# Kernel tuning notes

Measured on AMD Instinct MI355X. Metric: run time of the kernel, lower is better.

Reference implementation:

```python
import jax, jax.numpy as jnp
import numpy as np
import math

N_HEAD = 16
HEAD_DIM = 64
LN_EPS = 1e-5
TEMP = 1.0

def _layernorm(x, scale, bias):
    # normalize over last dim (head_dim)
    mu = jnp.mean(x, axis=-1, keepdims=True)
    var = jnp.mean(jnp.square(x - mu), axis=-1, keepdims=True)
    return (x - mu) / jnp.sqrt(var + LN_EPS) * scale + bias

def setup_inputs() -> dict:
    key = jax.random.key(0)
    ks = jax.random.split(key, 3)
    B, S, C = 4, 2048, 1024
    x = jax.random.normal(ks[0], (B, S, C), dtype=jnp.float32)
    w_qkv = jax.random.normal(ks[1], (C, 3 * C), dtype=jnp.float32) * (C ** -0.5)
    w_proj = jax.random.normal(ks[2], (C, C), dtype=jnp.float32) * (C ** -0.5)
    return {
        "x": x,
        "w_qkv": w_qkv,
        "w_proj": w_proj,
        "q_scale": jnp.ones((HEAD_DIM,), jnp.float32),
        "q_bias": jnp.zeros((HEAD_DIM,), jnp.float32),
        "k_scale": jnp.ones((HEAD_DIM,), jnp.float32),
        "k_bias": jnp.zeros((HEAD_DIM,), jnp.float32),
    }

def reference(x, w_qkv, w_proj, q_scale, q_bias, k_scale, k_bias):
    B, S, C = x.shape
    H, D = N_HEAD, HEAD_DIM
    # qkv projection -> [B,S,3,H,D] -> [3,B,H,S,D]
    qkv = (x @ w_qkv).reshape(B, S, 3, H, D).transpose(2, 0, 3, 1, 4)
    q = _layernorm(qkv[0], q_scale, q_bias)
    k = _layernorm(qkv[1], k_scale, k_bias)
    v = qkv[2]
    # temperature-scaled logits, stable softmax
    inv = 1.0 / (math.sqrt(D) * max(TEMP, 1e-6))
    logits = jnp.einsum('bhqd,bhkd->bhqk', q, k) * inv
    att = jax.nn.softmax(logits, axis=-1)
    # entropy stats (track_stats=True path)
    s_raw = -jnp.sum(att * jnp.log(att + 1e-9), axis=-1)  # [B,H,S]
    batch_entropies = jnp.mean(s_raw / math.log(S), axis=(1, 2))  # [B]
    out = jnp.einsum('bhqk,bhkd->bhqd', att, v).transpose(0, 2, 1, 3).reshape(B, S, C)
    return out @ w_proj, batch_entropies
```

## Files before the change

kernel.cpp:

```cpp
#include <hip/hip_runtime.h>
#include <hip/hip_bf16.h>
#include <math.h>

#define CB 4
#define CS 2048
#define CC 1024
#define CH 16
#define CD 64
#define CBS (CB*CS)

typedef unsigned short u16;
typedef __bf16 bf16x8 __attribute__((ext_vector_type(8)));
typedef float f32x4 __attribute__((ext_vector_type(4)));
typedef float f32x16 __attribute__((ext_vector_type(16)));
typedef unsigned short u16x4 __attribute__((ext_vector_type(4)));
typedef unsigned short u16x8 __attribute__((ext_vector_type(8)));
typedef unsigned u32x2 __attribute__((ext_vector_type(2)));

__device__ __forceinline__ u16 f2bf(float f){
  union { float f; unsigned u; } v; v.f = f;
  unsigned r = v.u + 0x7FFFu + ((v.u >> 16) & 1u);
  return (u16)(r >> 16);
}
__device__ __forceinline__ unsigned pack2bf(float a, float b){
  __hip_bfloat162 h = __float22bfloat162_rn(make_float2(a, b));
  union { __hip_bfloat162 h; unsigned u; } c; c.h = h; return c.u;
}
__device__ __forceinline__ f32x4 mfma16(bf16x8 a, bf16x8 b, f32x4 c){
  return __builtin_amdgcn_mfma_f32_16x16x32_bf16(a, b, c, 0, 0, 0);
}
__device__ __forceinline__ f32x16 mfma32(bf16x8 a, bf16x8 b, f32x16 c){
  return __builtin_amdgcn_mfma_f32_32x32x16_bf16(a, b, c, 0, 0, 0);
}
__device__ __forceinline__ void gload16(const u16* g, u16* lds_base_uniform){
  __builtin_amdgcn_global_load_lds(
      (const __attribute__((address_space(1))) unsigned int*)g,
      (__attribute__((address_space(3))) unsigned int*)lds_base_uniform, 16, 0, 0);
}

__global__ __launch_bounds__(256) void convert_x_kernel(
    const float* __restrict__ x, u16* __restrict__ xb, float* __restrict__ zero4){
  if (blockIdx.x == 0 && threadIdx.x < 4) zero4[threadIdx.x] = 0.0f;
  size_t i = ((size_t)blockIdx.x*256 + threadIdx.x)*8;
  float4 a = *(const float4*)(x+i);
  float4 b = *(const float4*)(x+i+4);
  u16x8 o = { f2bf(a.x),f2bf(a.y),f2bf(a.z),f2bf(a.w),
              f2bf(b.x),f2bf(b.y),f2bf(b.z),f2bf(b.w) };
  *(u16x8*)(xb+i) = o;
}

template<int K, int N>
__global__ __launch_bounds__(256) void transpose_convert_kernel(
    const float* __restrict__ w, u16* __restrict__ wt){
  __shared__ u16 tile[64][65];
  const int nb = N/64;
  int tk0 = (blockIdx.x / nb) * 64;
  int tn0 = (blockIdx.x % nb) * 64;
  int t = threadIdx.x;
  for (int i = 0; i < 4; i++) {
    int r = i*16 + (t>>4);
    int c = (t&15)*4;
    float4 v = *(const float4*)(w + (size_t)(tk0+r)*N + tn0 + c);
    tile[c+0][r]=f2bf(v.x); tile[c+1][r]=f2bf(v.y);
    tile[c+2][r]=f2bf(v.z); tile[c+3][r]=f2bf(v.w);
  }
  __syncthreads();
  for (int i = 0; i < 4; i++) {
    int r = i*16 + (t>>4);
    int c = (t&15)*4;
    u16x4 o = { tile[r][c+0], tile[r][c+1], tile[r][c+2], tile[r][c+3] };
    *(u16x4*)(wt + (size_t)(tn0+r)*K + tk0 + c) = o;
  }
}

__global__ __launch_bounds__(256) void transpose_v_kernel(
    const u16* __restrict__ vb, u16* __restrict__ vtb){
  __shared__ u16 tile[64][72];
  int bh = blockIdx.x >> 5;
  int st = blockIdx.x & 31;
  int t = threadIdx.x;
  const u16* src = vb + (size_t)bh*CS*CD + (size_t)st*64*CD;
  int r = t>>2, c = (t&3)*16;
  *(u16x8*)&tile[r][c]   = *(const u16x8*)(src + (size_t)r*CD + c);
  *(u16x8*)&tile[r][c+8] = *(const u16x8*)(src + (size_t)r*CD + c + 8);
  __syncthreads();
  int d = t>>2, s = (t&3)*16;
  u16x8 o0, o1;
  for (int j=0;j<8;j++){ o0[j] = tile[s+j][d]; o1[j] = tile[s+8+j][d]; }
  u16* dst = vtb + (size_t)bh*CD*CS + (size_t)d*CS + st*64 + s;
  *(u16x8*)dst = o0;
  *(u16x8*)(dst+8) = o1;
}

__global__ __launch_bounds__(256, 3) void gemm_qkv_ln_kernel(
    const u16* __restrict__ xb, const u16* __restrict__ wqkvT,
    const float* __restrict__ qsc, const float* __restrict__ qbi,
    const float* __restrict__ ksc, const float* __restrict__ kbi,
    u16* __restrict__ qb, u16* __restrict__ kb, u16* __restrict__ vb){
  __shared__ __align__(16) u16 bl[3][128*32];
  int t = threadIdx.x;
  int wv = t >> 6, lane = t & 63, lo = lane & 15, q4 = lane >> 4;
  int m0 = blockIdx.x * 128;
  int n0 = blockIdx.y * 128;
  int lsB = (lane & 3) ^ ((lane >> 3) & 3);
  const u16* bg0  = wqkvT + (size_t)(n0 + (lane>>2))*CC + lsB*8;
  const u16* agl0 = xb + (size_t)(m0 + wv*32 + lo)*CC + q4*8;
  const u16* agl1 = agl0 + (size_t)16*CC;

  f32x4 acc[2][8];
  #pragma unroll
  for (int i=0;i<2;i++)
    #pragma unroll
    for (int j=0;j<8;j++) acc[i][j] = (f32x4){0.f,0.f,0.f,0.f};

  auto stageB = [&](int buf, int kk){
    #pragma unroll
    for (int cc=0; cc<2; cc++){
      int c = wv*2 + cc;
      gload16(bg0 + (size_t)c*16*CC + kk*32, &bl[buf][c*512]);
    }
  };

  stageB(0, 0);
  stageB(1, 1);
  bf16x8 acur0 = *(const bf16x8*)(agl0);
  bf16x8 acur1 = *(const bf16x8*)(agl1);
  int cur = 0;
  const int akey = (lo >> 1) & 3;

  for (int kk = 0; kk < 32; kk++){
    if (kk < 30){
      asm volatile("s_waitcnt vmcnt(4)" ::: "memory");
      __builtin_amdgcn_s_barrier();
      __builtin_amdgcn_sched_barrier(0);
      int nb = cur + 2; if (nb >= 3) nb -= 3;
      stageB(nb, kk + 2);
    } else if (kk == 30){
      asm volatile("s_waitcnt vmcnt(4)" ::: "memory");
      __builtin_amdgcn_s_barrier();
      __builtin_amdgcn_sched_barrier(0);
    } else {
      asm volatile("s_waitcnt vmcnt(0)" ::: "memory");
      __builtin_amdgcn_s_barrier();
      __builtin_amdgcn_sched_barrier(0);
    }
    bf16x8 anxt0, anxt1;
    if (kk < 31){
      anxt0 = *(const bf16x8*)(agl0 + (kk+1)*32);
      anxt1 = *(const bf16x8*)(agl1 + (kk+1)*32);
    } else {
      anxt0 = acur0; anxt1 = acur1;
    }
    const u16* bc = &bl[cur][0];
    int soff = (q4 ^ akey) << 3;
    __builtin_amdgcn_s_setprio(1);
    #pragma unroll
    for (int nt=0; nt<8; nt++){
      bf16x8 b = *(const bf16x8*)&bc[(nt*16 + lo)*32 + soff];
      acc[0][nt] = mfma16(acur0, b, acc[0][nt]);
      acc[1][nt] = mfma16(acur1, b, acc[1][nt]);
    }
    __builtin_amdgcn_s_setprio(0);
    acur0 = anxt0; acur1 = anxt1;
    cur = (cur == 2) ? 0 : cur + 1;
  }

  int three = n0 >> 10;
  int h0 = (n0 & 1023) >> 6;
  const float* scp = (three == 0) ? qsc : ksc;
  const float* bip = (three == 0) ? qbi : kbi;
  float outscale = (three == 0) ? 0.125f * 1.44269504088896f : 1.0f;
  u16* dst = (three == 0) ? qb : (three == 1 ? kb : vb);

  for (int rt = 0; rt < 2; rt++){
    int tg = m0 + wv*32 + rt*16 + q4*4;
    for (int hf = 0; hf < 2; hf++){
      int h = h0 + hf;
      for (int r = 0; r < 4; r++){
        int token = tg + r;
        int bb = token >> 11, ss = token & (CS-1);
        size_t base = (((size_t)(bb*CH + h))*CS + ss)*CD;
        if (three < 2){
          float s1 = 0.f, s2 = 0.f;
          for (int j=0;j<4;j++){ float v = acc[rt][hf*4+j][r]; s1 += v; s2 += v*v; }
          for (int off=8; off>=1; off>>=1){
            s1 += __shfl_xor(s1, off, 16);
            s2 += __shfl_xor(s2, off, 16);
          }
          float mean = s1 * (1.f/64.f);
          float var  = s2 * (1.f/64.f) - mean*mean;
          float rstd = rsqrtf(var + 1e-5f);
          for (int j=0;j<4;j++){
            int d = j*16 + lo;
            float v = (acc[rt][hf*4+j][r] - mean) * rstd * scp[d] + bip[d];
            dst[base + d] = f2bf(v * outscale);
          }
        } else {
          for (int j=0;j<4;j++){
            int d = j*16 + lo;
            dst[base + d] = f2bf(acc[rt][hf*4+j][r]);
          }
        }
      }
    }
  }
}

__global__ __launch_bounds__(256, 2) void attention_kernel(
    const u16* __restrict__ qb, const u16* __restrict__ kb,
    const u16* __restrict__ vtb, u16* __restrict__ attnb, float* __restrict__ ent){
  __shared__ __align__(16) u16 kl[3][32*64];
  __shared__ __align__(16) u16 vl[3][64*32];
  int t = threadIdx.x;
  int wv = t >> 6, lane = t & 63;
  int col = lane & 31, hi = lane >> 5;
  int n = blockIdx.x;
  int xc = n & 7, j = n >> 3;
  int bh = xc + 8*(j >> 4);
  int qt = j & 15;
  int bI = bh >> 4;
  int q0w = qt*128 + wv*32;
  const u16* qbp = qb  + (size_t)bh * CS * CD;
  const u16* kbp = kb  + (size_t)bh * CS * CD;
  const u16* vbp = vtb + (size_t)bh * CD * CS;

  int srow8  = lane >> 3, sl8 = lane & 7;
  int srow16 = lane >> 2, sl4 = lane & 3;

  bf16x8 qf[4];
  #pragma unroll
  for (int ks=0;ks<4;ks++)
    qf[ks] = *(const bf16x8*)(qbp + (size_t)(q0w + col)*CD + ks*16 + hi*8);

  f32x16 o[2];
  #pragma unroll
  for (int nt=0;nt<2;nt++)
    #pragma unroll
    for (int i=0;i<16;i++) o[nt][i] = 0.f;
  float zacc = 0.f, tacc = 0.f;

  auto stage = [&](int buf, int tile){
    int skn = tile*32;
    int krow  = wv*8 + srow8;
    int kslot = sl8 ^ srow8 ^ wv;
    gload16(kbp + (size_t)(skn + krow)*CD + kslot*8, &kl[buf][wv*512]);
    int vrow  = wv*16 + srow16;
    int vslot = sl4 ^ (srow16 & 3);
    gload16(vbp + (size_t)vrow*CS + skn + vslot*8, &vl[buf][wv*512]);
  };

  stage(0, 0);
  stage(1, 1);

  const int kkey = (col & 7) ^ (col >> 3);
  const int vkey = (col & 3);
  int cur = 0;

  for (int it = 0; it < 64; it++){
    if (it < 62){
      asm volatile("s_waitcnt vmcnt(2)" ::: "memory");
      __builtin_amdgcn_s_barrier();
      __builtin_amdgcn_sched_barrier(0);
      int nb = cur + 2; if (nb >= 3) nb -= 3;
      stage(nb, it + 2);
    } else if (it == 62){
      asm volatile("s_waitcnt vmcnt(2)" ::: "memory");
      __builtin_amdgcn_s_barrier();
      __builtin_amdgcn_sched_barrier(0);
    } else {
      asm volatile("s_waitcnt vmcnt(0)" ::: "memory");
      __builtin_amdgcn_s_barrier();
      __builtin_amdgcn_sched_barrier(0);
    }
    const u16* kc = &kl[cur][0];
    const u16* vc = &vl[cur][0];

    bf16x8 kfr[4], vfr[2][2];
    #pragma unroll
    for (int ks=0;ks<4;ks++)
      kfr[ks] = *(const bf16x8*)&kc[col*64 + (((2*ks+hi) ^ kkey)<<3)];
    #pragma unroll
    for (int nt=0;nt<2;nt++)
      #pragma unroll
      for (int ks=0;ks<2;ks++)
        vfr[nt][ks] = *(const bf16x8*)&vc[(nt*32+col)*32 + (((ks*2+hi) ^ vkey)<<3)];

    f32x16 sf;
    #pragma unroll
    for (int i=0;i<16;i++) sf[i] = 0.f;
    __builtin_amdgcn_s_setprio(1);
    #pragma unroll
    for (int ks=0;ks<4;ks++)
      sf = mfma32(kfr[ks], qf[ks], sf);
    __builtin_amdgcn_s_setprio(0);

    #pragma unroll
    for (int ksl=0; ksl<2; ksl++){
      float p[2][4];
      #pragma unroll
      for (int gg=0; gg<2; gg++){
        int g = 2*ksl + gg;
        float l0 = sf[g*4+0], l1 = sf[g*4+1],
              l2 = sf[g*4+2], l3 = sf[g*4+3];
        float p0 = __builtin_amdgcn_exp2f(l0);
        float p1 = __builtin_amdgcn_exp2f(l1);
        float p2 = __builtin_amdgcn_exp2f(l2);
        float p3 = __builtin_amdgcn_exp2f(l3);
        zacc += (p0+p1)+(p2+p3);
        tacc += (p0*l0+p1*l1)+(p2*l2+p3*l3);
        p[gg][0]=p0; p[gg][1]=p1; p[gg][2]=p2; p[gg][3]=p3;
      }
      unsigned x0 = pack2bf(p[0][0], p[0][1]);
      unsigned x1 = pack2bf(p[0][2], p[0][3]);
      unsigned y0 = pack2bf(p[1][0], p[1][1]);
      unsigned y1 = pack2bf(p[1][2], p[1][3]);
      u32x2 s0 = __builtin_amdgcn_permlane32_swap(x0, y0, false, false);
      u32x2 s1 = __builtin_amdgcn_permlane32_swap(x1, y1, false, false);
      union { unsigned u[4]; bf16x8 v; } ap;
      ap.u[0] = s0[0]; ap.u[1] = s1[0]; ap.u[2] = s0[1]; ap.u[3] = s1[1];
      __builtin_amdgcn_s_setprio(1);
      o[0] = mfma32(ap.v, vfr[0][ksl], o[0]);
      o[1] = mfma32(ap.v, vfr[1][ksl], o[1]);
      __builtin_amdgcn_s_setprio(0);
    }
    cur = (cur == 2) ? 0 : cur + 1;
  }

  float z2 = zacc + __shfl_xor(zacc, 32);
  float t2 = tacc + __shfl_xor(tacc, 32);
  float invz = 1.f / z2;

  float srowv = 0.69314718055995f * (__builtin_amdgcn_logf(z2) - t2 * invz);
  float ev = (hi == 0) ? srowv : 0.f;
  for (int off=1; off<=32; off<<=1) ev += __shfl_xor(ev, off);
  if (lane == 0){
    float entscale = 1.0f / ((float)CH * (float)CS * logf((float)CS));
    atomicAdd(&ent[bI], ev * entscale);
  }

  float izv[4][4];
  #pragma unroll
  for (int g=0; g<4; g++)
    #pragma unroll
    for (int r=0; r<4; r++)
      izv[g][r] = __shfl(invz, 8*g + 4*hi + r);

  u16* obase = attnb + ((size_t)bh*CS + q0w)*CD;
  #pragma unroll
  for (int nt=0;nt<2;nt++){
    #pragma unroll
    for (int g=0;g<4;g++){
      #pragma unroll
      for (int r=0;r<4;r++){
        int qrow = 8*g + 4*hi + r;
        obase[(size_t)qrow*CD + nt*32 + col] = f2bf(o[nt][g*4+r] * izv[g][r]);
      }
    }
  }
}

__global__ __launch_bounds__(256, 3) void gemm_out_kernel(
    const u16* __restrict__ attnH, const u16* __restrict__ wprojT,
    float* __restrict__ out){
  __shared__ __align__(16) u16 bl[3][128*32];
  int t = threadIdx.x;
  int wv = t >> 6, lane = t & 63, lo = lane & 15, q4 = lane >> 4;
  int m0 = blockIdx.x * 128;
  int n0 = blockIdx.y * 128;
  int b  = m0 >> 11, s0 = m0 & (CS-1);
  int lsB = (lane & 3) ^ ((lane >> 3) & 3);
  const u16* bg0 = wprojT + (size_t)(n0 + (lane>>2))*CC + lsB*8;
  const u16* agl0 = attnH + ((size_t)(b*CH)*CS + s0 + wv*32 + lo)*CD + q4*8;
  const u16* agl1 = agl0 + (size_t)16*CD;

  f32x4 acc[2][8];
  #pragma unroll
  for (int i=0;i<2;i++)
    #pragma unroll
    for (int j=0;j<8;j++) acc[i][j] = (f32x4){0.f,0.f,0.f,0.f};

  auto aoff = [&](int kk) -> size_t {
    return (size_t)(kk >> 1)*CS*CD + (size_t)(kk & 1)*32;
  };
  auto stageB = [&](int buf, int kk){
    #pragma unroll
    for (int cc=0; cc<2; cc++){
      int c = wv*2 + cc;
      gload16(bg0 + (size_t)c*16*CC + kk*32, &bl[buf][c*512]);
    }
  };

  stageB(0, 0);
  stageB(1, 1);
  bf16x8 acur0 = *(const bf16x8*)(agl0);
  bf16x8 acur1 = *(const bf16x8*)(agl1);
  int cur = 0;
  const int akey = (lo >> 1) & 3;

  for (int kk = 0; kk < 32; kk++){
    if (kk < 30){
      asm volatile("s_waitcnt vmcnt(4)" ::: "memory");
      __builtin_amdgcn_s_barrier();
      __builtin_amdgcn_sched_barrier(0);
      int nb = cur + 2; if (nb >= 3) nb -= 3;
      stageB(nb, kk + 2);
    } else if (kk == 30){
      asm volatile("s_waitcnt vmcnt(4)" ::: "memory");
      __builtin_amdgcn_s_barrier();
      __builtin_amdgcn_sched_barrier(0);
    } else {
      asm volatile("s_waitcnt vmcnt(0)" ::: "memory");
      __builtin_amdgcn_s_barrier();
      __builtin_amdgcn_sched_barrier(0);
    }
    bf16x8 anxt0, anxt1;
    if (kk < 31){
      size_t ao = aoff(kk + 1);
      anxt0 = *(const bf16x8*)(agl0 + ao);
      anxt1 = *(const bf16x8*)(agl1 + ao);
    } else {
      anxt0 = acur0; anxt1 = acur1;
    }
    const u16* bc = &bl[cur][0];
    int soff = (q4 ^ akey) << 3;
    __builtin_amdgcn_s_setprio(1);
    #pragma unroll
    for (int nt=0; nt<8; nt++){
      bf16x8 b2 = *(const bf16x8*)&bc[(nt*16 + lo)*32 + soff];
      acc[0][nt] = mfma16(acur0, b2, acc[0][nt]);
      acc[1][nt] = mfma16(acur1, b2, acc[1][nt]);
    }
    __builtin_amdgcn_s_setprio(0);
    acur0 = anxt0; acur1 = anxt1;
    cur = (cur == 2) ? 0 : cur + 1;
  }

  for (int rt=0;rt<2;rt++){
    for (int r=0;r<4;r++){
      int row = m0 + wv*32 + rt*16 + q4*4 + r;
      for (int nt=0;nt<8;nt++)
        out[(size_t)row*CC + n0 + nt*16 + lo] = acc[rt][nt][r];
    }
  }
}

extern "C" void kernel_launch(void* const* d_in, const int* in_sizes, int n_in,
                              void* d_out, int out_size, void* d_ws, size_t ws_size,
                              hipStream_t stream) {
  const float* x      = (const float*)d_in[0];
  const float* w_qkv  = (const float*)d_in[1];
  const float* w_proj = (const float*)d_in[2];
  const float* q_scale= (const float*)d_in[3];
  const float* q_bias = (const float*)d_in[4];
  const float* k_scale= (const float*)d_in[5];
  const float* k_bias = (const float*)d_in[6];
  float* out = (float*)d_out;
  float* ent = out + (size_t)CBS * CC;

  u16* xb     = (u16*)d_ws;
  u16* wqkvT  = xb     + (size_t)CBS*CC;
  u16* wprojT = wqkvT  + (size_t)3*CC*CC;
  u16* qb     = wprojT + (size_t)CC*CC;
  u16* kb     = qb + (size_t)CB*CH*CS*CD;
  u16* vb     = kb + (size_t)CB*CH*CS*CD;
  u16* vbT    = xb;
  u16* attn   = vb;

  convert_x_kernel<<<dim3(CBS*CC/(256*8)), 256, 0, stream>>>(x, xb, ent);
  transpose_convert_kernel<CC, 3*CC><<<dim3((CC/64)*(3*CC/64)), 256, 0, stream>>>(w_qkv, wqkvT);
  transpose_convert_kernel<CC, CC><<<dim3((CC/64)*(CC/64)), 256, 0, stream>>>(w_proj, wprojT);
  gemm_qkv_ln_kernel<<<dim3(CBS/128, 3*CC/128), 256, 0, stream>>>(
      xb, wqkvT, q_scale, q_bias, k_scale, k_bias, qb, kb, vb);
  transpose_v_kernel<<<dim3(CB*CH*(CS/64)), 256, 0, stream>>>(vb, vbT);
  attention_kernel<<<dim3(CB*CH*(CS/128)), 256, 0, stream>>>(qb, kb, vbT, attn, ent);
  gemm_out_kernel<<<dim3(CBS/128, CC/128), 256, 0, stream>>>(attn, wprojT, out);
}
```

Baseline: 332.8 us.

## Enlarge GEMM M-tile to 256 rows per block in QKV and output projections

Both projection GEMMs now compute 256x128 tiles instead of 128x128, with each wave holding four 16-row A fragments and 4x8 accumulators. Each B tile staged in shared memory is reused across twice as many MFMAs, which cuts LDS B traffic and global B loads per FLOP. The waitcnt thresholds are adjusted for the extra in-flight A loads, and launch bounds drop to 2 blocks per CU to allow the higher register use. The grid is halved, which reduces occupancy and the number of blocks available to fill the GPU.

After: 347.5 us. 1.04x slower.

```diff
diff --git a/kernel.cpp b/kernel.cpp
--- a/kernel.cpp
+++ b/kernel.cpp
@@ -92,7 +92,7 @@
   *(u16x8*)(dst+8) = o1;
 }
 
-__global__ __launch_bounds__(256, 3) void gemm_qkv_ln_kernel(
+__global__ __launch_bounds__(256, 2) void gemm_qkv_ln_kernel(
     const u16* __restrict__ xb, const u16* __restrict__ wqkvT,
     const float* __restrict__ qsc, const float* __restrict__ qbi,
     const float* __restrict__ ksc, const float* __restrict__ kbi,
@@ -100,16 +100,18 @@
   __shared__ __align__(16) u16 bl[3][128*32];
   int t = threadIdx.x;
   int wv = t >> 6, lane = t & 63, lo = lane & 15, q4 = lane >> 4;
-  int m0 = blockIdx.x * 128;
+  int m0 = blockIdx.x * 256;
   int n0 = blockIdx.y * 128;
   int lsB = (lane & 3) ^ ((lane >> 3) & 3);
-  const u16* bg0  = wqkvT + (size_t)(n0 + (lane>>2))*CC + lsB*8;
-  const u16* agl0 = xb + (size_t)(m0 + wv*32 + lo)*CC + q4*8;
-  const u16* agl1 = agl0 + (size_t)16*CC;
-
-  f32x4 acc[2][8];
-  #pragma unroll
-  for (int i=0;i<2;i++)
+  const u16* bg0 = wqkvT + (size_t)(n0 + (lane>>2))*CC + lsB*8;
+  const u16* agl[4];
+  #pragma unroll
+  for (int g=0; g<4; g++)
+    agl[g] = xb + (size_t)(m0 + wv*64 + g*16 + lo)*CC + q4*8;
+
+  f32x4 acc[4][8];
+  #pragma unroll
+  for (int i=0;i<4;i++)
     #pragma unroll
     for (int j=0;j<8;j++) acc[i][j] = (f32x4){0.f,0.f,0.f,0.f};
 
@@ -123,33 +125,35 @@
 
   stageB(0, 0);
   stageB(1, 1);
-  bf16x8 acur0 = *(const bf16x8*)(agl0);
-  bf16x8 acur1 = *(const bf16x8*)(agl1);
+  bf16x8 acur[4];
+  #pragma unroll
+  for (int g=0; g<4; g++) acur[g] = *(const bf16x8*)(agl[g]);
   int cur = 0;
   const int akey = (lo >> 1) & 3;
 
   for (int kk = 0; kk < 32; kk++){
     if (kk < 30){
-      asm volatile("s_waitcnt vmcnt(4)" ::: "memory");
+      asm volatile("s_waitcnt vmcnt(6)" ::: "memory");
       __builtin_amdgcn_s_barrier();
       __builtin_amdgcn_sched_barrier(0);
       int nb = cur + 2; if (nb >= 3) nb -= 3;
       stageB(nb, kk + 2);
     } else if (kk == 30){
+      asm volatile("s_waitcnt vmcnt(6)" ::: "memory");
+      __builtin_amdgcn_s_barrier();
+      __builtin_amdgcn_sched_barrier(0);
+    } else {
       asm volatile("s_waitcnt vmcnt(4)" ::: "memory");
       __builtin_amdgcn_s_barrier();
       __builtin_amdgcn_sched_barrier(0);
+    }
+    bf16x8 anxt[4];
+    if (kk < 31){
+      #pragma unroll
+      for (int g=0; g<4; g++) anxt[g] = *(const bf16x8*)(agl[g] + (kk+1)*32);
     } else {
-      asm volatile("s_waitcnt vmcnt(0)" ::: "memory");
-      __builtin_amdgcn_s_barrier();
-      __builtin_amdgcn_sched_barrier(0);
-    }
-    bf16x8 anxt0, anxt1;
-    if (kk < 31){
-      anxt0 = *(const bf16x8*)(agl0 + (kk+1)*32);
-      anxt1 = *(const bf16x8*)(agl1 + (kk+1)*32);
-    } else {
-      anxt0 = acur0; anxt1 = acur1;
+      #pragma unroll
+      for (int g=0; g<4; g++) anxt[g] = acur[g];
     }
     const u16* bc = &bl[cur][0];
     int soff = (q4 ^ akey) << 3;
@@ -157,11 +161,14 @@
     #pragma unroll
     for (int nt=0; nt<8; nt++){
       bf16x8 b = *(const bf16x8*)&bc[(nt*16 + lo)*32 + soff];
-      acc[0][nt] = mfma16(acur0, b, acc[0][nt]);
-      acc[1][nt] = mfma16(acur1, b, acc[1][nt]);
+      acc[0][nt] = mfma16(acur[0], b, acc[0][nt]);
+      acc[1][nt] = mfma16(acur[1], b, acc[1][nt]);
+      acc[2][nt] = mfma16(acur[2], b, acc[2][nt]);
+      acc[3][nt] = mfma16(acur[3], b, acc[3][nt]);
     }
     __builtin_amdgcn_s_setprio(0);
-    acur0 = anxt0; acur1 = anxt1;
+    #pragma unroll
+    for (int g=0; g<4; g++) acur[g] = anxt[g];
     cur = (cur == 2) ? 0 : cur + 1;
   }
 
@@ -172,8 +179,8 @@
   float outscale = (three == 0) ? 0.125f * 1.44269504088896f : 1.0f;
   u16* dst = (three == 0) ? qb : (three == 1 ? kb : vb);
 
-  for (int rt = 0; rt < 2; rt++){
-    int tg = m0 + wv*32 + rt*16 + q4*4;
+  for (int rt = 0; rt < 4; rt++){
+    int tg = m0 + wv*64 + rt*16 + q4*4;
     for (int hf = 0; hf < 2; hf++){
       int h = h0 + hf;
       for (int r = 0; r < 4; r++){
@@ -359,23 +366,25 @@
   }
 }
 
-__global__ __launch_bounds__(256, 3) void gemm_out_kernel(
+__global__ __launch_bounds__(256, 2) void gemm_out_kernel(
     const u16* __restrict__ attnH, const u16* __restrict__ wprojT,
     float* __restrict__ out){
   __shared__ __align__(16) u16 bl[3][128*32];
   int t = threadIdx.x;
   int wv = t >> 6, lane = t & 63, lo = lane & 15, q4 = lane >> 4;
-  int m0 = blockIdx.x * 128;
+  int m0 = blockIdx.x * 256;
   int n0 = blockIdx.y * 128;
   int b  = m0 >> 11, s0 = m0 & (CS-1);
   int lsB = (lane & 3) ^ ((lane >> 3) & 3);
   const u16* bg0 = wprojT + (size_t)(n0 + (lane>>2))*CC + lsB*8;
-  const u16* agl0 = attnH + ((size_t)(b*CH)*CS + s0 + wv*32 + lo)*CD + q4*8;
-  const u16* agl1 = agl0 + (size_t)16*CD;
-
-  f32x4 acc[2][8];
-  #pragma unroll
-  for (int i=0;i<2;i++)
+  const u16* agl[4];
+  #pragma unroll
+  for (int g=0; g<4; g++)
+    agl[g] = attnH + ((size_t)(b*CH)*CS + s0 + wv*64 + g*16 + lo)*CD + q4*8;
+
+  f32x4 acc[4][8];
+  #pragma unroll
+  for (int i=0;i<4;i++)
     #pragma unroll
     for (int j=0;j<8;j++) acc[i][j] = (f32x4){0.f,0.f,0.f,0.f};
 
@@ -392,34 +401,36 @@
 
   stageB(0, 0);
   stageB(1, 1);
-  bf16x8 acur0 = *(const bf16x8*)(agl0);
-  bf16x8 acur1 = *(const bf16x8*)(agl1);
+  bf16x8 acur[4];
+  #pragma unroll
+  for (int g=0; g<4; g++) acur[g] = *(const bf16x8*)(agl[g]);
   int cur = 0;
   const int akey = (lo >> 1) & 3;
 
   for (int kk = 0; kk < 32; kk++){
     if (kk < 30){
-      asm volatile("s_waitcnt vmcnt(4)" ::: "memory");
+      asm volatile("s_waitcnt vmcnt(6)" ::: "memory");
       __builtin_amdgcn_s_barrier();
       __builtin_amdgcn_sched_barrier(0);
       int nb = cur + 2; if (nb >= 3) nb -= 3;
       stageB(nb, kk + 2);
     } else if (kk == 30){
+      asm volatile("s_waitcnt vmcnt(6)" ::: "memory");
+      __builtin_amdgcn_s_barrier();
+      __builtin_amdgcn_sched_barrier(0);
+    } else {
       asm volatile("s_waitcnt vmcnt(4)" ::: "memory");
       __builtin_amdgcn_s_barrier();
       __builtin_amdgcn_sched_barrier(0);
-    } else {
-      asm volatile("s_waitcnt vmcnt(0)" ::: "memory");
-      __builtin_amdgcn_s_barrier();
-      __builtin_amdgcn_sched_barrier(0);
-    }
-    bf16x8 anxt0, anxt1;
+    }
+    bf16x8 anxt[4];
     if (kk < 31){
       size_t ao = aoff(kk + 1);
-      anxt0 = *(const bf16x8*)(agl0 + ao);
-      anxt1 = *(const bf16x8*)(agl1 + ao);
+      #pragma unroll
+      for (int g=0; g<4; g++) anxt[g] = *(const bf16x8*)(agl[g] + ao);
     } else {
-      anxt0 = acur0; anxt1 = acur1;
+      #pragma unroll
+      for (int g=0; g<4; g++) anxt[g] = acur[g];
     }
     const u16* bc = &bl[cur][0];
     int soff = (q4 ^ akey) << 3;
@@ -427,17 +438,20 @@
     #pragma unroll
     for (int nt=0; nt<8; nt++){
       bf16x8 b2 = *(const bf16x8*)&bc[(nt*16 + lo)*32 + soff];
-      acc[0][nt] = mfma16(acur0, b2, acc[0][nt]);
-      acc[1][nt] = mfma16(acur1, b2, acc[1][nt]);
+      acc[0][nt] = mfma16(acur[0], b2, acc[0][nt]);
+      acc[1][nt] = mfma16(acur[1], b2, acc[1][nt]);
+      acc[2][nt] = mfma16(acur[2], b2, acc[2][nt]);
+      acc[3][nt] = mfma16(acur[3], b2, acc[3][nt]);
     }
     __builtin_amdgcn_s_setprio(0);
-    acur0 = anxt0; acur1 = anxt1;
+    #pragma unroll
+    for (int g=0; g<4; g++) acur[g] = anxt[g];
     cur = (cur == 2) ? 0 : cur + 1;
   }
 
-  for (int rt=0;rt<2;rt++){
+  for (int rt=0;rt<4;rt++){
     for (int r=0;r<4;r++){
-      int row = m0 + wv*32 + rt*16 + q4*4 + r;
+      int row = m0 + wv*64 + rt*16 + q4*4 + r;
       for (int nt=0;nt<8;nt++)
         out[(size_t)row*CC + n0 + nt*16 + lo] = acc[rt][nt][r];
     }
@@ -469,9 +483,9 @@
   convert_x_kernel<<<dim3(CBS*CC/(256*8)), 256, 0, stream>>>(x, xb, ent);
   transpose_convert_kernel<CC, 3*CC><<<dim3((CC/64)*(3*CC/64)), 256, 0, stream>>>(w_qkv, wqkvT);
   transpose_convert_kernel<CC, CC><<<dim3((CC/64)*(CC/64)), 256, 0, stream>>>(w_proj, wprojT);
-  gemm_qkv_ln_kernel<<<dim3(CBS/128, 3*CC/128), 256, 0, stream>>>(
+  gemm_qkv_ln_kernel<<<dim3(CBS/256, 3*CC/128), 256, 0, stream>>>(
       xb, wqkvT, q_scale, q_bias, k_scale, k_bias, qb, kb, vb);
   transpose_v_kernel<<<dim3(CB*CH*(CS/64)), 256, 0, stream>>>(vb, vbT);
   attention_kernel<<<dim3(CB*CH*(CS/128)), 256, 0, stream>>>(qb, kb, vbT, attn, ent);
-  gemm_out_kernel<<<dim3(CBS/128, CC/128), 256, 0, stream>>>(attn, wprojT, out);
-}
+  gemm_out_kernel<<<dim3(CBS/256, CC/128), 256, 0, stream>>>(attn, wprojT, out);
+}
```

## Run attention as single-wave blocks with private double-buffered K/V staging, no barriers

Applied to the files above, without the earlier changes.

Each attention block now holds a single 64-thread wave that handles 32 queries, instead of four waves sharing K/V tiles. Every wave stages its own K and V tiles into a double buffer, so the block-wide barriers and the triple-buffer rotation go away; waitcnt on vmem and lgkm is enough to order the loads. In exchange, K/V traffic from global/L2 grows roughly four-fold because tiles are no longer shared across waves, and the grid gets four times as many blocks.

After: 355.0 us. 1.07x slower.

```diff
diff --git a/kernel.cpp b/kernel.cpp
--- a/kernel.cpp
+++ b/kernel.cpp
@@ -206,47 +206,52 @@
   }
 }
 
-__global__ __launch_bounds__(256, 2) void attention_kernel(
+__global__ __launch_bounds__(64, 2) void attention_kernel(
     const u16* __restrict__ qb, const u16* __restrict__ kb,
     const u16* __restrict__ vtb, u16* __restrict__ attnb, float* __restrict__ ent){
-  __shared__ __align__(16) u16 kl[3][32*64];
-  __shared__ __align__(16) u16 vl[3][64*32];
-  int t = threadIdx.x;
-  int wv = t >> 6, lane = t & 63;
+  __shared__ __align__(16) u16 kl[2][32*64];
+  __shared__ __align__(16) u16 vl[2][64*32];
+  int lane = threadIdx.x & 63;
   int col = lane & 31, hi = lane >> 5;
   int n = blockIdx.x;
   int xc = n & 7, j = n >> 3;
-  int bh = xc + 8*(j >> 4);
-  int qt = j & 15;
+  int qt = j & 63;
+  int bh = xc + 8*(j >> 6);
   int bI = bh >> 4;
-  int q0w = qt*128 + wv*32;
+  int q0w = qt*32;
   const u16* qbp = qb  + (size_t)bh * CS * CD;
   const u16* kbp = kb  + (size_t)bh * CS * CD;
   const u16* vbp = vtb + (size_t)bh * CD * CS;
 
+  bf16x8 qf[4];
+  #pragma unroll
+  for (int ks=0;ks<4;ks++)
+    qf[ks] = *(const bf16x8*)(qbp + (size_t)(q0w + col)*CD + ks*16 + hi*8);
+
+  f32x16 o[2];
+  #pragma unroll
+  for (int nt=0;nt<2;nt++)
+    #pragma unroll
+    for (int i=0;i<16;i++) o[nt][i] = 0.f;
+  float zacc = 0.f, tacc = 0.f;
+
   int srow8  = lane >> 3, sl8 = lane & 7;
   int srow16 = lane >> 2, sl4 = lane & 3;
 
-  bf16x8 qf[4];
-  #pragma unroll
-  for (int ks=0;ks<4;ks++)
-    qf[ks] = *(const bf16x8*)(qbp + (size_t)(q0w + col)*CD + ks*16 + hi*8);
-
-  f32x16 o[2];
-  #pragma unroll
-  for (int nt=0;nt<2;nt++)
-    #pragma unroll
-    for (int i=0;i<16;i++) o[nt][i] = 0.f;
-  float zacc = 0.f, tacc = 0.f;
-
-  auto stage = [&](int buf, int tile){
+  auto stage = [&](int b, int tile){
     int skn = tile*32;
-    int krow  = wv*8 + srow8;
-    int kslot = sl8 ^ srow8 ^ wv;
-    gload16(kbp + (size_t)(skn + krow)*CD + kslot*8, &kl[buf][wv*512]);
-    int vrow  = wv*16 + srow16;
-    int vslot = sl4 ^ (srow16 & 3);
-    gload16(vbp + (size_t)vrow*CS + skn + vslot*8, &vl[buf][wv*512]);
+    #pragma unroll
+    for (int c=0;c<4;c++){
+      int kr = c*8 + srow8;
+      int ks_ = sl8 ^ srow8 ^ c;
+      gload16(kbp + (size_t)(skn + kr)*CD + ks_*8, &kl[b][c*512]);
+    }
+    #pragma unroll
+    for (int c=0;c<4;c++){
+      int vr = c*16 + srow16;
+      int vs = sl4 ^ (srow16 & 3);
+      gload16(vbp + (size_t)vr*CS + skn + vs*8, &vl[b][c*512]);
+    }
   };
 
   stage(0, 0);
@@ -254,24 +259,14 @@
 
   const int kkey = (col & 7) ^ (col >> 3);
   const int vkey = (col & 3);
-  int cur = 0;
 
   for (int it = 0; it < 64; it++){
-    if (it < 62){
-      asm volatile("s_waitcnt vmcnt(2)" ::: "memory");
-      __builtin_amdgcn_s_barrier();
-      __builtin_amdgcn_sched_barrier(0);
-      int nb = cur + 2; if (nb >= 3) nb -= 3;
-      stage(nb, it + 2);
-    } else if (it == 62){
-      asm volatile("s_waitcnt vmcnt(2)" ::: "memory");
-      __builtin_amdgcn_s_barrier();
-      __builtin_amdgcn_sched_barrier(0);
+    if (it < 63){
+      asm volatile("s_waitcnt vmcnt(8)" ::: "memory");
     } else {
       asm volatile("s_waitcnt vmcnt(0)" ::: "memory");
-      __builtin_amdgcn_s_barrier();
-      __builtin_amdgcn_sched_barrier(0);
-    }
+    }
+    const int cur = it & 1;
     const u16* kc = &kl[cur][0];
     const u16* vc = &vl[cur][0];
 
@@ -284,6 +279,10 @@
       #pragma unroll
       for (int ks=0;ks<2;ks++)
         vfr[nt][ks] = *(const bf16x8*)&vc[(nt*32+col)*32 + (((ks*2+hi) ^ vkey)<<3)];
+
+    asm volatile("s_waitcnt lgkmcnt(0)" ::: "memory");
+    __builtin_amdgcn_sched_barrier(0);
+    if (it < 62) stage(cur, it + 2);
 
     f32x16 sf;
     #pragma unroll
@@ -323,7 +322,6 @@
       o[1] = mfma32(ap.v, vfr[1][ksl], o[1]);
       __builtin_amdgcn_s_setprio(0);
     }
-    cur = (cur == 2) ? 0 : cur + 1;
   }
 
   float z2 = zacc + __shfl_xor(zacc, 32);
@@ -472,6 +470,6 @@
   gemm_qkv_ln_kernel<<<dim3(CBS/128, 3*CC/128), 256, 0, stream>>>(
       xb, wqkvT, q_scale, q_bias, k_scale, k_bias, qb, kb, vb);
   transpose_v_kernel<<<dim3(CB*CH*(CS/64)), 256, 0, stream>>>(vb, vbT);
-  attention_kernel<<<dim3(CB*CH*(CS/128)), 256, 0, stream>>>(qb, kb, vbT, attn, ent);
+  attention_kernel<<<dim3(CB*CH*(CS/32)), 64, 0, stream>>>(qb, kb, vbT, attn, ent);
   gemm_out_kernel<<<dim3(CBS/128, CC/128), 256, 0, stream>>>(attn, wprojT, out);
 }
```
